# Kernel optimization log

Hardware: AMD Instinct MI355X
Metric: run time of the kernel (lower is better)

The kernel has to match this reference:

```python
import jax, jax.numpy as jnp
import numpy as np

N = 50000      # nodes
E = 400000     # edges (before self loops)
IN = 128       # in_feat
HID = 64       # n_hidden per head
HEADS = [4, 4, 1]
NEG_SLOPE = 0.2  # DGL GATConv default


def gat_layer(h, src, dst, W, al, ar, b, n_nodes):
    # h: [N, Din]; W: [Din, H*F]; al/ar: [H, F]; b: [H*F]
    H, F = al.shape
    feat = (h @ W).reshape(n_nodes, H, F)              # [N,H,F]
    el = jnp.sum(feat * al, axis=-1)                   # [N,H]
    er = jnp.sum(feat * ar, axis=-1)                   # [N,H]
    e = jax.nn.leaky_relu(el[src] + er[dst], NEG_SLOPE)  # [E,H]
    # edge softmax over destination node segments (stable)
    e_max = jax.lax.stop_gradient(jax.ops.segment_max(e, dst, num_segments=n_nodes))
    ex = jnp.exp(e - e_max[dst])                       # [E,H]
    denom = jax.ops.segment_sum(ex, dst, num_segments=n_nodes)  # [N,H]
    alpha = ex / denom[dst]                            # [E,H]
    msg = feat[src] * alpha[:, :, None]                # [E,H,F]
    out = jax.ops.segment_sum(msg, dst, num_segments=n_nodes)   # [N,H,F]
    out = out + b.reshape(1, H, F)
    return out.reshape(n_nodes, H * F)


def setup_inputs() -> dict:
    key = jax.random.key(0)
    ks = jax.random.split(key, 16)
    inp = {
        "node_feat": jax.random.normal(ks[0], (N, IN), jnp.float32),
        "src": jax.random.randint(ks[1], (E,), 0, N),
        "dst": jax.random.randint(ks[2], (E,), 0, N),
    }
    dins = [IN, HID * HEADS[0], HID * HEADS[1]]
    for i, (din, h) in enumerate(zip(dins, HEADS)):
        k = 3 + 3 * i
        inp[f"W{i}"] = jax.random.normal(ks[k], (din, h * HID), jnp.float32) * 0.1
        inp[f"al{i}"] = jax.random.normal(ks[k + 1], (h, HID), jnp.float32) * 0.1
        inp[f"ar{i}"] = jax.random.normal(ks[k + 2], (h, HID), jnp.float32) * 0.1
        inp[f"b{i}"] = jnp.zeros((h * HID,), jnp.float32)
    return inp


def reference(node_feat, src, dst, W0, al0, ar0, b0, W1, al1, ar1, b1, W2, al2, ar2, b2):
    n_nodes = node_feat.shape[0]
    # add_self_loop
    loop = jnp.arange(n_nodes, dtype=src.dtype)
    src_a = jnp.concatenate([src, loop])
    dst_a = jnp.concatenate([dst, loop])
    h = node_feat
    h = gat_layer(h, src_a, dst_a, W0, al0, ar0, b0, n_nodes)  # [N, 4*64]
    h = gat_layer(h, src_a, dst_a, W1, al1, ar1, b1, n_nodes)  # [N, 4*64]
    h = gat_layer(h, src_a, dst_a, W2, al2, ar2, b2, n_nodes)  # [N, 64]
    return h
```

## Files before the change

### kernel.cpp

```cpp
#include <hip/hip_runtime.h>


typedef __attribute__((ext_vector_type(8))) short short8;
typedef __attribute__((ext_vector_type(4))) float f32x4;
typedef __attribute__((ext_vector_type(4))) int int4v;

__device__ __forceinline__ float bf2f(ushort u) {
  union { unsigned int i; float f; } c;
  c.i = ((unsigned int)u) << 16;
  return c.f;
}
__device__ __forceinline__ ushort f2bf(float f) {
  union { float f; unsigned int i; } c;
  c.f = f;
  unsigned int u = c.i;
  u += 0x7FFFu + ((u >> 16) & 1u);
  return (ushort)(u >> 16);
}
__device__ __forceinline__ float lrelu_exp(float x) {
  const float y = fmaxf(x, 0.2f * x);
  return __expf(y);
}
__device__ __forceinline__ void gload_lds16(const ushort* g, void* lds) {
  __builtin_amdgcn_global_load_lds(
      (const __attribute__((address_space(1))) unsigned int*)g,
      (__attribute__((address_space(3))) unsigned int*)lds, 16, 0, 0);
}

__global__ __launch_bounds__(256) void prep_kernel(
    const float* __restrict__ nf, ushort* __restrict__ a0, int n8, int nbA,
    const float* __restrict__ W0, ushort* __restrict__ Wt0,
    const float* __restrict__ W1, ushort* __restrict__ Wt1,
    const float* __restrict__ W2, ushort* __restrict__ Wt2, int nbW,
    int* __restrict__ cnt, int Nn, int nbZ, ushort* __restrict__ feat_sent,
    float* __restrict__ el4, float* __restrict__ el1) {
  const int b = blockIdx.x;
  if (b < nbA) {
    const int i = b * 256 + threadIdx.x;
    if (i >= n8) return;
    const float4 v0 = ((const float4*)nf)[i * 2];
    const float4 v1 = ((const float4*)nf)[i * 2 + 1];
    short8 o;
    o[0] = (short)f2bf(v0.x); o[1] = (short)f2bf(v0.y);
    o[2] = (short)f2bf(v0.z); o[3] = (short)f2bf(v0.w);
    o[4] = (short)f2bf(v1.x); o[5] = (short)f2bf(v1.y);
    o[6] = (short)f2bf(v1.z); o[7] = (short)f2bf(v1.w);
    ((short8*)a0)[i] = o;
  } else if (b < nbA + nbW) {
    const int i = (b - nbA) * 256 + threadIdx.x;
    if (i < 32768) {
      const int k = i >> 8, n = i & 255;
      Wt0[n * 128 + k] = f2bf(W0[i]);
    } else if (i < 32768 + 65536) {
      const int j = i - 32768;
      const int k = j >> 8, n = j & 255;
      Wt1[n * 256 + k] = f2bf(W1[j]);
    } else if (i < 32768 + 65536 + 16384) {
      const int j = i - 32768 - 65536;
      const int k = j >> 6, n = j & 63;
      Wt2[n * 256 + k] = f2bf(W2[j]);
    }
  } else if (b < nbA + nbW + nbZ) {
    const int idx = (b - nbA - nbW) * 256 + threadIdx.x;
    const int base = idx * 4;
    if (base + 4 <= Nn) {
      ((int4v*)cnt)[idx] = (int4v)0;
    } else if (base < Nn) {
      for (int j = base; j < Nn; ++j) cnt[j] = 0;
    }
  } else {
    const int t = threadIdx.x;
    if (t < 128) ((uint*)feat_sent)[t] = 0u;
    if (t >= 128 && t < 132) el4[(size_t)Nn * 4 + (t - 128)] = -1e9f;
    if (t == 132) el1[Nn] = -1e9f;
  }
}

template <int BN, bool FUSE>
__global__ __launch_bounds__(256) void gemm_mfma(
    const ushort* __restrict__ A, const ushort* __restrict__ Wt,
    ushort* __restrict__ C, int M, int K, int Nc,
    const float* __restrict__ al, const float* __restrict__ ar,
    float* __restrict__ el, float* __restrict__ er) {
  constexpr int NF = BN / 32;
  constexpr int NCHB = BN / 8;
  __shared__ ushort As[128][64];
  __shared__ ushort Bs[BN][64];
  const int bm = blockIdx.x * 128;
  const int bn = blockIdx.y * BN;
  const int tid = threadIdx.x;
  const int lane = tid & 63;
  const int wave = tid >> 6;
  const int wm = wave >> 1;
  const int wn = wave & 1;
  const int lrow = lane >> 3;
  const int lslot = lane & 7;

  f32x4 acc[4][NF];
#pragma unroll
  for (int m = 0; m < 4; ++m)
#pragma unroll
    for (int n = 0; n < NF; ++n) acc[m][n] = 0.f;

  for (int k0 = 0; k0 < K; k0 += 64) {
#pragma unroll
    for (int c = wave; c < 16; c += 4) {
      const int row = c * 8 + lrow;
      int rg = bm + row;
      if (rg >= M) rg = M - 1;
      const int kcol = (lslot ^ (row & 7)) * 8;
      gload_lds16(A + (size_t)rg * K + k0 + kcol,
                  (char*)(&As[0][0]) + c * 1024 + lrow * 128 + lslot * 16);
    }
#pragma unroll
    for (int c = wave; c < NCHB; c += 4) {
      const int row = c * 8 + lrow;
      const int kcol = (lslot ^ (row & 7)) * 8;
      gload_lds16(Wt + (size_t)(bn + row) * K + k0 + kcol,
                  (char*)(&Bs[0][0]) + c * 1024 + lrow * 128 + lslot * 16);
    }
    __syncthreads();

#pragma unroll
    for (int kk = 0; kk < 2; ++kk) {
      short8 a[4], b[NF];
#pragma unroll
      for (int m = 0; m < 4; ++m) {
        const int row = wm * 64 + m * 16 + (lane & 15);
        const int slot = (kk * 4 + (lane >> 4)) ^ (row & 7);
        a[m] = *(const short8*)((const char*)&As[0][0] + row * 128 + slot * 16);
      }
#pragma unroll
      for (int n = 0; n < NF; ++n) {
        const int row = wn * (NF * 16) + n * 16 + (lane & 15);
        const int slot = (kk * 4 + (lane >> 4)) ^ (row & 7);
        b[n] = *(const short8*)((const char*)&Bs[0][0] + row * 128 + slot * 16);
      }
#pragma unroll
      for (int m = 0; m < 4; ++m)
#pragma unroll
        for (int n = 0; n < NF; ++n)
          acc[m][n] = __builtin_amdgcn_mfma_f32_16x16x32_bf16(
              a[m], b[n], acc[m][n], 0, 0, 0);
    }
    __syncthreads();
  }

#pragma unroll
  for (int m = 0; m < 4; ++m) {
#pragma unroll
    for (int r = 0; r < 4; ++r) {
      const int row = bm + wm * 64 + m * 16 + (lane >> 4) * 4 + r;
      if (row < M) {
#pragma unroll
        for (int n = 0; n < NF; ++n) {
          const int col = bn + wn * (NF * 16) + n * 16 + (lane & 15);
          C[(size_t)row * Nc + col] = f2bf(acc[m][n][r]);
        }
      }
    }
  }

  if constexpr (FUSE) {
    const int cc = lane & 15;
    const int head = blockIdx.y * 2 + wn;
    float alv[NF], arv[NF];
#pragma unroll
    for (int n = 0; n < NF; ++n) {
      alv[n] = al[head * 64 + n * 16 + cc];
      arv[n] = ar[head * 64 + n * 16 + cc];
    }
#pragma unroll
    for (int m = 0; m < 4; ++m) {
#pragma unroll
      for (int r = 0; r < 4; ++r) {
        float pl = 0.f, pr = 0.f;
#pragma unroll
        for (int n = 0; n < NF; ++n) {
          pl = fmaf(acc[m][n][r], alv[n], pl);
          pr = fmaf(acc[m][n][r], arv[n], pr);
        }
#pragma unroll
        for (int o = 1; o < 16; o <<= 1) {
          pl += __shfl_xor(pl, o);
          pr += __shfl_xor(pr, o);
        }
        if (cc == 0) {
          const int row = bm + wm * 64 + m * 16 + (lane >> 4) * 4 + r;
          if (row < M) {
            el[row * 4 + head] = pl;
            er[row * 4 + head] = pr;
          }
        }
      }
    }
  }
}

__global__ __launch_bounds__(256) void attn_coef_h1(
    const ushort* __restrict__ feat, const float* __restrict__ al,
    const float* __restrict__ ar, float* __restrict__ el,
    float* __restrict__ er, int Nn) {
  const int wid = (blockIdx.x * 256 + threadIdx.x) >> 6;
  const int lane = threadIdx.x & 63;
  const int n = wid * 4 + (lane >> 4);
  const int sub = lane & 15;
  if (n >= Nn) return;
  const short4 v = ((const short4*)(feat + (size_t)n * 64))[sub];
  const float4 a = ((const float4*)al)[sub];
  const float4 r = ((const float4*)ar)[sub];
  const float f0 = bf2f((ushort)v.x), f1 = bf2f((ushort)v.y),
              f2 = bf2f((ushort)v.z), f3 = bf2f((ushort)v.w);
  float pl = f0 * a.x + f1 * a.y + f2 * a.z + f3 * a.w;
  float pr = f0 * r.x + f1 * r.y + f2 * r.z + f3 * r.w;
#pragma unroll
  for (int off = 1; off < 16; off <<= 1) {
    pl += __shfl_xor(pl, off);
    pr += __shfl_xor(pr, off);
  }
  if (sub == 0) {
    el[n] = pl;
    er[n] = pr;
  }
}

__global__ void hist_kernel(const int* __restrict__ dst, int* __restrict__ cnt,
                            int E, int Nn) {
  const int e = blockIdx.x * blockDim.x + threadIdx.x;
  if (e >= E + Nn) return;
  const int d = (e < E) ? dst[e] : (e - E);
  atomicAdd(&cnt[d], 1);
}

__device__ __forceinline__ int block_incl_scan_1024(int x, int* lds16) {
  const int lane = threadIdx.x & 63;
  const int wid = threadIdx.x >> 6;
  int inc = x;
#pragma unroll
  for (int off = 1; off < 64; off <<= 1) {
    const int y = __shfl_up(inc, off);
    if (lane >= off) inc += y;
  }
  if (lane == 63) lds16[wid] = inc;
  __syncthreads();
  if (wid == 0) {
    int t = (lane < 16) ? lds16[lane] : 0;
#pragma unroll
    for (int off = 1; off < 16; off <<= 1) {
      const int y = __shfl_up(t, off);
      if (lane >= off) t += y;
    }
    if (lane < 16) lds16[lane] = t;
  }
  __syncthreads();
  if (wid > 0) inc += lds16[wid - 1];
  return inc;
}

__global__ __launch_bounds__(1024) void scan_blocks_kernel(
    const int* __restrict__ cnt, int* __restrict__ row_ptr,
    int* __restrict__ partials, int n) {
  __shared__ int lds16[16];
  const int i = blockIdx.x * 1024 + threadIdx.x;
  const int x = (i < n) ? ((cnt[i] + 3) & ~3) : 0;
  const int inc = block_incl_scan_1024(x, lds16);
  if (i < n) row_ptr[i] = inc - x;
  if (threadIdx.x == 1023) partials[blockIdx.x] = inc;
}

__global__ __launch_bounds__(1024) void scan_partials_kernel(
    int* __restrict__ partials, int* __restrict__ row_ptr, int nb, int n) {
  __shared__ int lds16[16];
  const int x = (threadIdx.x < nb) ? partials[threadIdx.x] : 0;
  const int inc = block_incl_scan_1024(x, lds16);
  if (threadIdx.x < nb) partials[threadIdx.x] = inc - x;
  if (threadIdx.x == nb - 1) row_ptr[n] = inc;
}

__global__ __launch_bounds__(1024) void add_offsets_kernel(
    int* __restrict__ row_ptr, int* __restrict__ cursor,
    const int* __restrict__ partials, int n) {
  const int i = blockIdx.x * 1024 + threadIdx.x;
  if (i < n) {
    const int v = row_ptr[i] + partials[blockIdx.x];
    row_ptr[i] = v;
    cursor[i] = v;
  }
}

__global__ void scatter_kernel(const int* __restrict__ src,
                               const int* __restrict__ dst,
                               int* __restrict__ cursor, int* __restrict__ esrc,
                               int E, int Nn) {
  const int e = blockIdx.x * blockDim.x + threadIdx.x;
  if (e >= E + Nn) return;
  const int s = (e < E) ? src[e] : (e - E);
  const int d = (e < E) ? dst[e] : (e - E);
  const int pos = atomicAdd(&cursor[d], 1);
  esrc[pos] = s;
}

__global__ void fill_pad_kernel(const int* __restrict__ cursor,
                                const int* __restrict__ row_ptr,
                                int* __restrict__ esrc, int Nn) {
  const int n = blockIdx.x * 256 + threadIdx.x;
  if (n >= Nn) return;
  const int end = row_ptr[n + 1];
  for (int p = cursor[n]; p < end; ++p) esrc[p] = Nn;
}

__global__ __launch_bounds__(256) void agg_fused_h4(
    const int* __restrict__ row_ptr, const int* __restrict__ esrc,
    const float* __restrict__ el, const float* __restrict__ er,
    const ushort* __restrict__ feat, const float* __restrict__ b,
    ushort* __restrict__ out, int Nn) {
  const int n = (blockIdx.x * 256 + threadIdx.x) >> 6;
  const int lane = threadIdx.x & 63;
  if (n >= Nn) return;
  const int h = lane >> 4;
  int i = row_ptr[n];
  const int end = row_ptr[n + 1];
  const float erv = er[n * 4 + h];
  const short4* fb = (const short4*)feat + lane;

  float den = 0.f;
  f32x4 acc = 0.f;
  int s0 = esrc[i], s1 = esrc[i + 1], s2 = esrc[i + 2], s3 = esrc[i + 3];
  float x0 = el[s0 * 4 + h], x1 = el[s1 * 4 + h], x2 = el[s2 * 4 + h],
        x3 = el[s3 * 4 + h];
  short4 f0 = fb[(size_t)s0 * 64], f1 = fb[(size_t)s1 * 64],
         f2 = fb[(size_t)s2 * 64], f3 = fb[(size_t)s3 * 64];
  for (i += 4; i < end; i += 4) {
    const int t0 = esrc[i], t1 = esrc[i + 1], t2 = esrc[i + 2],
              t3 = esrc[i + 3];
    const float y0 = el[t0 * 4 + h], y1 = el[t1 * 4 + h], y2 = el[t2 * 4 + h],
                y3 = el[t3 * 4 + h];
    const short4 g0 = fb[(size_t)t0 * 64], g1 = fb[(size_t)t1 * 64],
                 g2 = fb[(size_t)t2 * 64], g3 = fb[(size_t)t3 * 64];
    const float e0 = lrelu_exp(x0 + erv), e1 = lrelu_exp(x1 + erv),
                e2 = lrelu_exp(x2 + erv), e3 = lrelu_exp(x3 + erv);
    den += (e0 + e1) + (e2 + e3);
    acc[0] += e0 * bf2f((ushort)f0.x) + e1 * bf2f((ushort)f1.x) +
              e2 * bf2f((ushort)f2.x) + e3 * bf2f((ushort)f3.x);
    acc[1] += e0 * bf2f((ushort)f0.y) + e1 * bf2f((ushort)f1.y) +
              e2 * bf2f((ushort)f2.y) + e3 * bf2f((ushort)f3.y);
    acc[2] += e0 * bf2f((ushort)f0.z) + e1 * bf2f((ushort)f1.z) +
              e2 * bf2f((ushort)f2.z) + e3 * bf2f((ushort)f3.z);
    acc[3] += e0 * bf2f((ushort)f0.w) + e1 * bf2f((ushort)f1.w) +
              e2 * bf2f((ushort)f2.w) + e3 * bf2f((ushort)f3.w);
    x0 = y0; x1 = y1; x2 = y2; x3 = y3;
    f0 = g0; f1 = g1; f2 = g2; f3 = g3;
  }
  {
    const float e0 = lrelu_exp(x0 + erv), e1 = lrelu_exp(x1 + erv),
                e2 = lrelu_exp(x2 + erv), e3 = lrelu_exp(x3 + erv);
    den += (e0 + e1) + (e2 + e3);
    acc[0] += e0 * bf2f((ushort)f0.x) + e1 * bf2f((ushort)f1.x) +
              e2 * bf2f((ushort)f2.x) + e3 * bf2f((ushort)f3.x);
    acc[1] += e0 * bf2f((ushort)f0.y) + e1 * bf2f((ushort)f1.y) +
              e2 * bf2f((ushort)f2.y) + e3 * bf2f((ushort)f3.y);
    acc[2] += e0 * bf2f((ushort)f0.z) + e1 * bf2f((ushort)f1.z) +
              e2 * bf2f((ushort)f2.z) + e3 * bf2f((ushort)f3.z);
    acc[3] += e0 * bf2f((ushort)f0.w) + e1 * bf2f((ushort)f1.w) +
              e2 * bf2f((ushort)f2.w) + e3 * bf2f((ushort)f3.w);
  }
  const float rden = 1.f / den;
  const float4 bb = ((const float4*)b)[lane];
  short4 o;
  o.x = (short)f2bf(acc[0] * rden + bb.x);
  o.y = (short)f2bf(acc[1] * rden + bb.y);
  o.z = (short)f2bf(acc[2] * rden + bb.z);
  o.w = (short)f2bf(acc[3] * rden + bb.w);
  ((short4*)out)[(size_t)n * 64 + lane] = o;
}

__global__ __launch_bounds__(256) void agg_fused_h1(
    const int* __restrict__ row_ptr, const int* __restrict__ esrc,
    const float* __restrict__ el, const float* __restrict__ er,
    const ushort* __restrict__ feat, const float* __restrict__ b,
    float* __restrict__ out, int Nn) {
  const int wid = (blockIdx.x * 256 + threadIdx.x) >> 6;
  const int lane = threadIdx.x & 63;
  const int n = wid * 2 + (lane >> 5);
  const int sub = lane & 31;
  if (n >= Nn) return;
  int i = row_ptr[n];
  const int end = row_ptr[n + 1];
  const float erv = er[n];
  const uint* fb = (const uint*)feat + sub;

  float den = 0.f;
  float a0 = 0.f, a1 = 0.f;
  int s0 = esrc[i], s1 = esrc[i + 1], s2 = esrc[i + 2], s3 = esrc[i + 3];
  float x0 = el[s0], x1 = el[s1], x2 = el[s2], x3 = el[s3];
  uint f0 = fb[(size_t)s0 * 32], f1 = fb[(size_t)s1 * 32],
       f2 = fb[(size_t)s2 * 32], f3 = fb[(size_t)s3 * 32];
  for (i += 4; i < end; i += 4) {
    const int t0 = esrc[i], t1 = esrc[i + 1], t2 = esrc[i + 2],
              t3 = esrc[i + 3];
    const float y0 = el[t0], y1 = el[t1], y2 = el[t2], y3 = el[t3];
    const uint g0 = fb[(size_t)t0 * 32], g1 = fb[(size_t)t1 * 32],
               g2 = fb[(size_t)t2 * 32], g3 = fb[(size_t)t3 * 32];
    const float e0 = lrelu_exp(x0 + erv), e1 = lrelu_exp(x1 + erv),
                e2 = lrelu_exp(x2 + erv), e3 = lrelu_exp(x3 + erv);
    den += (e0 + e1) + (e2 + e3);
    a0 += e0 * bf2f((ushort)(f0 & 0xffff)) + e1 * bf2f((ushort)(f1 & 0xffff)) +
          e2 * bf2f((ushort)(f2 & 0xffff)) + e3 * bf2f((ushort)(f3 & 0xffff));
    a1 += e0 * bf2f((ushort)(f0 >> 16)) + e1 * bf2f((ushort)(f1 >> 16)) +
          e2 * bf2f((ushort)(f2 >> 16)) + e3 * bf2f((ushort)(f3 >> 16));
    x0 = y0; x1 = y1; x2 = y2; x3 = y3;
    f0 = g0; f1 = g1; f2 = g2; f3 = g3;
  }
  {
    const float e0 = lrelu_exp(x0 + erv), e1 = lrelu_exp(x1 + erv),
                e2 = lrelu_exp(x2 + erv), e3 = lrelu_exp(x3 + erv);
    den += (e0 + e1) + (e2 + e3);
    a0 += e0 * bf2f((ushort)(f0 & 0xffff)) + e1 * bf2f((ushort)(f1 & 0xffff)) +
          e2 * bf2f((ushort)(f2 & 0xffff)) + e3 * bf2f((ushort)(f3 & 0xffff));
    a1 += e0 * bf2f((ushort)(f0 >> 16)) + e1 * bf2f((ushort)(f1 >> 16)) +
          e2 * bf2f((ushort)(f2 >> 16)) + e3 * bf2f((ushort)(f3 >> 16));
  }
  const float rden = 1.f / den;
  const float2 bb = ((const float2*)b)[sub];
  float2 o;
  o.x = a0 * rden + bb.x;
  o.y = a1 * rden + bb.y;
  ((float2*)out)[(size_t)n * 32 + sub] = o;
}

extern "C" void kernel_launch(void* const* d_in, const int* in_sizes, int n_in,
                              void* d_out, int out_size, void* d_ws,
                              size_t ws_size, hipStream_t stream) {
  const float* nf = (const float*)d_in[0];
  const int* src = (const int*)d_in[1];
  const int* dst = (const int*)d_in[2];
  const float* W0 = (const float*)d_in[3];
  const float* al0 = (const float*)d_in[4];
  const float* ar0 = (const float*)d_in[5];
  const float* b0 = (const float*)d_in[6];
  const float* W1 = (const float*)d_in[7];
  const float* al1 = (const float*)d_in[8];
  const float* ar1 = (const float*)d_in[9];
  const float* b1 = (const float*)d_in[10];
  const float* W2 = (const float*)d_in[11];
  const float* al2 = (const float*)d_in[12];
  const float* ar2 = (const float*)d_in[13];
  const float* b2 = (const float*)d_in[14];

  const int IN = 128;
  const int Nn = in_sizes[0] / IN;
  const int E = in_sizes[1];
  const int ETP = E + 4 * Nn;

  char* ws = (char*)d_ws;
  size_t off = 0;
  auto alloc = [&](size_t bytes) {
    char* p = ws + off;
    off += (bytes + 255) & ~(size_t)255;
    return p;
  };
  ushort* feat = (ushort*)alloc(((size_t)Nn + 1) * 256 * 2);
  ushort* h1 = (ushort*)alloc((size_t)Nn * 256 * 2);
  ushort* h2 = (ushort*)alloc((size_t)Nn * 256 * 2);
  ushort* a0 = (ushort*)alloc((size_t)Nn * 128 * 2);
  ushort* Wt0 = (ushort*)alloc((size_t)256 * 128 * 2);
  ushort* Wt1 = (ushort*)alloc((size_t)256 * 256 * 2);
  ushort* Wt2 = (ushort*)alloc((size_t)64 * 256 * 2);
  float* el4 = (float*)alloc(((size_t)Nn + 1) * 4 * 4);
  float* er4 = (float*)alloc((size_t)Nn * 4 * 4);
  float* el1 = (float*)alloc(((size_t)Nn + 1) * 4);
  float* er1 = (float*)alloc((size_t)Nn * 4);
  int* row_ptr = (int*)alloc(((size_t)Nn + 1) * 4);
  int* cnt = (int*)alloc((size_t)Nn * 4);
  int* cursor = (int*)alloc((size_t)Nn * 4);
  int* esrc = (int*)alloc((size_t)ETP * 4);
  int* partials = (int*)alloc((size_t)1024 * 4);
  (void)ws_size;
  (void)n_in;
  (void)out_size;

  const int n8 = Nn * 16;
  const int nbA = (n8 + 255) / 256;
  const int nbW = (32768 + 65536 + 16384 + 255) / 256;
  const int nbZ = (Nn + 1023) / 1024;
  prep_kernel<<<nbA + nbW + nbZ + 1, 256, 0, stream>>>(
      nf, a0, n8, nbA, W0, Wt0, W1, Wt1, W2, Wt2, nbW, cnt, Nn, nbZ,
      feat + (size_t)Nn * 256, el4, el1);

  const int ET = E + Nn;
  const int nb = (Nn + 1023) / 1024;
  hist_kernel<<<(ET + 255) / 256, 256, 0, stream>>>(dst, cnt, E, Nn);
  scan_blocks_kernel<<<nb, 1024, 0, stream>>>(cnt, row_ptr, partials, Nn);
  scan_partials_kernel<<<1, 1024, 0, stream>>>(partials, row_ptr, nb, Nn);
  add_offsets_kernel<<<nb, 1024, 0, stream>>>(row_ptr, cursor, partials, Nn);
  scatter_kernel<<<(ET + 255) / 256, 256, 0, stream>>>(src, dst, cursor, esrc,
                                                       E, Nn);
  fill_pad_kernel<<<(Nn + 255) / 256, 256, 0, stream>>>(cursor, row_ptr, esrc,
                                                        Nn);

  const int waves_grid = (Nn * 64 + 255) / 256;

  {
    dim3 gg((Nn + 127) / 128, 2);
    gemm_mfma<128, true><<<gg, 256, 0, stream>>>(a0, Wt0, feat, Nn, 128, 256,
                                                 al0, ar0, el4, er4);
    agg_fused_h4<<<waves_grid, 256, 0, stream>>>(row_ptr, esrc, el4, er4, feat,
                                                 b0, h1, Nn);
  }
  {
    dim3 gg((Nn + 127) / 128, 2);
    gemm_mfma<128, true><<<gg, 256, 0, stream>>>(h1, Wt1, feat, Nn, 256, 256,
                                                 al1, ar1, el4, er4);
    agg_fused_h4<<<waves_grid, 256, 0, stream>>>(row_ptr, esrc, el4, er4, feat,
                                                 b1, h2, Nn);
  }
  {
    dim3 gg((Nn + 127) / 128, 1);
    gemm_mfma<64, false><<<gg, 256, 0, stream>>>(h2, Wt2, feat, Nn, 256, 64,
                                                 nullptr, nullptr, nullptr,
                                                 nullptr);
    attn_coef_h1<<<(Nn * 16 + 255) / 256, 256, 0, stream>>>(feat, al2, ar2,
                                                            el1, er1, Nn);
    agg_fused_h1<<<(Nn * 32 + 255) / 256, 256, 0, stream>>>(
        row_ptr, esrc, el1, er1, feat, b2, (float*)d_out, Nn);
  }
}
```

Before: 211.8 us.

## Fuse layer-3 attention coefficients into GEMM, prefill padding, vectorize edge gathers

Three changes. The layer-3 attention coefficients (el/er) are now computed in the GEMM epilogue through an LDS reduction, which removes the attn_coef_h1 kernel. The padding slots in esrc are pre-filled with the sentinel node inside prep_kernel, which removes fill_pad_kernel. The aggregation loops now read edge sources as int4 groups of four and keep two groups in flight to hide more gather latency. Together these save two launches and issue fewer load instructions, at the cost of more registers per thread and an extra LDS sync in the GEMM.

```diff
diff --git a/kernel.cpp b/kernel.cpp
--- a/kernel.cpp
+++ b/kernel.cpp
@@ -32,8 +32,9 @@
     const float* __restrict__ W0, ushort* __restrict__ Wt0,
     const float* __restrict__ W1, ushort* __restrict__ Wt1,
     const float* __restrict__ W2, ushort* __restrict__ Wt2, int nbW,
-    int* __restrict__ cnt, int Nn, int nbZ, ushort* __restrict__ feat_sent,
-    float* __restrict__ el4, float* __restrict__ el1) {
+    int* __restrict__ cnt, int Nn, int nbZ, int* __restrict__ esrc, int ETP,
+    int nbE, ushort* __restrict__ feat_sent, float* __restrict__ el4,
+    float* __restrict__ el1) {
   const int b = blockIdx.x;
   if (b < nbA) {
     const int i = b * 256 + threadIdx.x;
@@ -68,6 +69,14 @@
     } else if (base < Nn) {
       for (int j = base; j < Nn; ++j) cnt[j] = 0;
     }
+  } else if (b < nbA + nbW + nbZ + nbE) {
+    const int idx = (b - nbA - nbW - nbZ) * 256 + threadIdx.x;
+    const int base = idx * 4;
+    if (base + 4 <= ETP) {
+      ((int4*)esrc)[idx] = make_int4(Nn, Nn, Nn, Nn);
+    } else if (base < ETP) {
+      for (int j = base; j < ETP; ++j) esrc[j] = Nn;
+    }
   } else {
     const int t = threadIdx.x;
     if (t < 128) ((uint*)feat_sent)[t] = 0u;
@@ -76,7 +85,7 @@
   }
 }
 
-template <int BN, bool FUSE>
+template <int BN, int FUSE>
 __global__ __launch_bounds__(256) void gemm_mfma(
     const ushort* __restrict__ A, const ushort* __restrict__ Wt,
     ushort* __restrict__ C, int M, int K, int Nc,
@@ -161,7 +170,7 @@
     }
   }
 
-  if constexpr (FUSE) {
+  if constexpr (FUSE == 1) {
     const int cc = lane & 15;
     const int head = blockIdx.y * 2 + wn;
     float alv[NF], arv[NF];
@@ -195,32 +204,47 @@
       }
     }
   }
-}
-
-__global__ __launch_bounds__(256) void attn_coef_h1(
-    const ushort* __restrict__ feat, const float* __restrict__ al,
-    const float* __restrict__ ar, float* __restrict__ el,
-    float* __restrict__ er, int Nn) {
-  const int wid = (blockIdx.x * 256 + threadIdx.x) >> 6;
-  const int lane = threadIdx.x & 63;
-  const int n = wid * 4 + (lane >> 4);
-  const int sub = lane & 15;
-  if (n >= Nn) return;
-  const short4 v = ((const short4*)(feat + (size_t)n * 64))[sub];
-  const float4 a = ((const float4*)al)[sub];
-  const float4 r = ((const float4*)ar)[sub];
-  const float f0 = bf2f((ushort)v.x), f1 = bf2f((ushort)v.y),
-              f2 = bf2f((ushort)v.z), f3 = bf2f((ushort)v.w);
-  float pl = f0 * a.x + f1 * a.y + f2 * a.z + f3 * a.w;
-  float pr = f0 * r.x + f1 * r.y + f2 * r.z + f3 * r.w;
-#pragma unroll
-  for (int off = 1; off < 16; off <<= 1) {
-    pl += __shfl_xor(pl, off);
-    pr += __shfl_xor(pr, off);
-  }
-  if (sub == 0) {
-    el[n] = pl;
-    er[n] = pr;
+
+  if constexpr (FUSE == 2) {
+    float* red = (float*)&As[0][0];
+    const int cc = lane & 15;
+    const int q = lane >> 4;
+    float alv[NF], arv[NF];
+#pragma unroll
+    for (int n = 0; n < NF; ++n) {
+      alv[n] = al[wn * (NF * 16) + n * 16 + cc];
+      arv[n] = ar[wn * (NF * 16) + n * 16 + cc];
+    }
+#pragma unroll
+    for (int m = 0; m < 4; ++m) {
+#pragma unroll
+      for (int r = 0; r < 4; ++r) {
+        float pl = 0.f, pr = 0.f;
+#pragma unroll
+        for (int n = 0; n < NF; ++n) {
+          pl = fmaf(acc[m][n][r], alv[n], pl);
+          pr = fmaf(acc[m][n][r], arv[n], pr);
+        }
+#pragma unroll
+        for (int o = 1; o < 16; o <<= 1) {
+          pl += __shfl_xor(pl, o);
+          pr += __shfl_xor(pr, o);
+        }
+        if (cc == 0) {
+          const int rl = wm * 64 + m * 16 + q * 4 + r;
+          red[rl * 2 + wn] = pl;
+          red[256 + rl * 2 + wn] = pr;
+        }
+      }
+    }
+    __syncthreads();
+    if (tid < 128) {
+      const int row = bm + tid;
+      if (row < M) {
+        el[row] = red[tid * 2] + red[tid * 2 + 1];
+        er[row] = red[256 + tid * 2] + red[256 + tid * 2 + 1];
+      }
+    }
   }
 }
 
@@ -300,13 +324,38 @@
   esrc[pos] = s;
 }
 
-__global__ void fill_pad_kernel(const int* __restrict__ cursor,
-                                const int* __restrict__ row_ptr,
-                                int* __restrict__ esrc, int Nn) {
-  const int n = blockIdx.x * 256 + threadIdx.x;
-  if (n >= Nn) return;
-  const int end = row_ptr[n + 1];
-  for (int p = cursor[n]; p < end; ++p) esrc[p] = Nn;
+struct G4h4 {
+  float x0, x1, x2, x3;
+  short4 f0, f1, f2, f3;
+};
+__device__ __forceinline__ G4h4 ld4_h4(const int* __restrict__ esrc, int p4,
+                                       const float* __restrict__ el, int h,
+                                       const short4* __restrict__ fb) {
+  const int4 s = *(const int4*)(esrc + (p4 << 2));
+  G4h4 g;
+  g.x0 = el[s.x * 4 + h];
+  g.x1 = el[s.y * 4 + h];
+  g.x2 = el[s.z * 4 + h];
+  g.x3 = el[s.w * 4 + h];
+  g.f0 = fb[(size_t)s.x * 64];
+  g.f1 = fb[(size_t)s.y * 64];
+  g.f2 = fb[(size_t)s.z * 64];
+  g.f3 = fb[(size_t)s.w * 64];
+  return g;
+}
+__device__ __forceinline__ void cp4_h4(const G4h4& g, float erv, float& den,
+                                       f32x4& acc) {
+  const float e0 = lrelu_exp(g.x0 + erv), e1 = lrelu_exp(g.x1 + erv),
+              e2 = lrelu_exp(g.x2 + erv), e3 = lrelu_exp(g.x3 + erv);
+  den += (e0 + e1) + (e2 + e3);
+  acc[0] += e0 * bf2f((ushort)g.f0.x) + e1 * bf2f((ushort)g.f1.x) +
+            e2 * bf2f((ushort)g.f2.x) + e3 * bf2f((ushort)g.f3.x);
+  acc[1] += e0 * bf2f((ushort)g.f0.y) + e1 * bf2f((ushort)g.f1.y) +
+            e2 * bf2f((ushort)g.f2.y) + e3 * bf2f((ushort)g.f3.y);
+  acc[2] += e0 * bf2f((ushort)g.f0.z) + e1 * bf2f((ushort)g.f1.z) +
+            e2 * bf2f((ushort)g.f2.z) + e3 * bf2f((ushort)g.f3.z);
+  acc[3] += e0 * bf2f((ushort)g.f0.w) + e1 * bf2f((ushort)g.f1.w) +
+            e2 * bf2f((ushort)g.f2.w) + e3 * bf2f((ushort)g.f3.w);
 }
 
 __global__ __launch_bounds__(256) void agg_fused_h4(
@@ -318,51 +367,35 @@
   const int lane = threadIdx.x & 63;
   if (n >= Nn) return;
   const int h = lane >> 4;
-  int i = row_ptr[n];
-  const int end = row_ptr[n + 1];
+  const int start = row_ptr[n];
+  const int g = (row_ptr[n + 1] - start) >> 2;
+  const int p = start >> 2;
   const float erv = er[n * 4 + h];
   const short4* fb = (const short4*)feat + lane;
 
   float den = 0.f;
   f32x4 acc = 0.f;
-  int s0 = esrc[i], s1 = esrc[i + 1], s2 = esrc[i + 2], s3 = esrc[i + 3];
-  float x0 = el[s0 * 4 + h], x1 = el[s1 * 4 + h], x2 = el[s2 * 4 + h],
-        x3 = el[s3 * 4 + h];
-  short4 f0 = fb[(size_t)s0 * 64], f1 = fb[(size_t)s1 * 64],
-         f2 = fb[(size_t)s2 * 64], f3 = fb[(size_t)s3 * 64];
-  for (i += 4; i < end; i += 4) {
-    const int t0 = esrc[i], t1 = esrc[i + 1], t2 = esrc[i + 2],
-              t3 = esrc[i + 3];
-    const float y0 = el[t0 * 4 + h], y1 = el[t1 * 4 + h], y2 = el[t2 * 4 + h],
-                y3 = el[t3 * 4 + h];
-    const short4 g0 = fb[(size_t)t0 * 64], g1 = fb[(size_t)t1 * 64],
-                 g2 = fb[(size_t)t2 * 64], g3 = fb[(size_t)t3 * 64];
-    const float e0 = lrelu_exp(x0 + erv), e1 = lrelu_exp(x1 + erv),
-                e2 = lrelu_exp(x2 + erv), e3 = lrelu_exp(x3 + erv);
-    den += (e0 + e1) + (e2 + e3);
-    acc[0] += e0 * bf2f((ushort)f0.x) + e1 * bf2f((ushort)f1.x) +
-              e2 * bf2f((ushort)f2.x) + e3 * bf2f((ushort)f3.x);
-    acc[1] += e0 * bf2f((ushort)f0.y) + e1 * bf2f((ushort)f1.y) +
-              e2 * bf2f((ushort)f2.y) + e3 * bf2f((ushort)f3.y);
-    acc[2] += e0 * bf2f((ushort)f0.z) + e1 * bf2f((ushort)f1.z) +
-              e2 * bf2f((ushort)f2.z) + e3 * bf2f((ushort)f3.z);
-    acc[3] += e0 * bf2f((ushort)f0.w) + e1 * bf2f((ushort)f1.w) +
-              e2 * bf2f((ushort)f2.w) + e3 * bf2f((ushort)f3.w);
-    x0 = y0; x1 = y1; x2 = y2; x3 = y3;
-    f0 = g0; f1 = g1; f2 = g2; f3 = g3;
-  }
-  {
-    const float e0 = lrelu_exp(x0 + erv), e1 = lrelu_exp(x1 + erv),
-                e2 = lrelu_exp(x2 + erv), e3 = lrelu_exp(x3 + erv);
-    den += (e0 + e1) + (e2 + e3);
-    acc[0] += e0 * bf2f((ushort)f0.x) + e1 * bf2f((ushort)f1.x) +
-              e2 * bf2f((ushort)f2.x) + e3 * bf2f((ushort)f3.x);
-    acc[1] += e0 * bf2f((ushort)f0.y) + e1 * bf2f((ushort)f1.y) +
-              e2 * bf2f((ushort)f2.y) + e3 * bf2f((ushort)f3.y);
-    acc[2] += e0 * bf2f((ushort)f0.z) + e1 * bf2f((ushort)f1.z) +
-              e2 * bf2f((ushort)f2.z) + e3 * bf2f((ushort)f3.z);
-    acc[3] += e0 * bf2f((ushort)f0.w) + e1 * bf2f((ushort)f1.w) +
-              e2 * bf2f((ushort)f2.w) + e3 * bf2f((ushort)f3.w);
+  G4h4 A = ld4_h4(esrc, p, el, h, fb);
+  if (g == 1) {
+    cp4_h4(A, erv, den, acc);
+  } else {
+    G4h4 B = ld4_h4(esrc, p + 1, el, h, fb);
+    int k = 2;
+    for (; k + 1 < g; k += 2) {
+      cp4_h4(A, erv, den, acc);
+      A = ld4_h4(esrc, p + k, el, h, fb);
+      cp4_h4(B, erv, den, acc);
+      B = ld4_h4(esrc, p + k + 1, el, h, fb);
+    }
+    if (k < g) {
+      cp4_h4(A, erv, den, acc);
+      A = ld4_h4(esrc, p + k, el, h, fb);
+      cp4_h4(B, erv, den, acc);
+      cp4_h4(A, erv, den, acc);
+    } else {
+      cp4_h4(A, erv, den, acc);
+      cp4_h4(B, erv, den, acc);
+    }
   }
   const float rden = 1.f / den;
   const float4 bb = ((const float4*)b)[lane];
@@ -372,6 +405,38 @@
   o.z = (short)f2bf(acc[2] * rden + bb.z);
   o.w = (short)f2bf(acc[3] * rden + bb.w);
   ((short4*)out)[(size_t)n * 64 + lane] = o;
+}
+
+struct G4h1 {
+  float x0, x1, x2, x3;
+  uint f0, f1, f2, f3;
+};
+__device__ __forceinline__ G4h1 ld4_h1(const int* __restrict__ esrc, int p4,
+                                       const float* __restrict__ el,
+                                       const uint* __restrict__ fb) {
+  const int4 s = *(const int4*)(esrc + (p4 << 2));
+  G4h1 g;
+  g.x0 = el[s.x];
+  g.x1 = el[s.y];
+  g.x2 = el[s.z];
+  g.x3 = el[s.w];
+  g.f0 = fb[(size_t)s.x * 32];
+  g.f1 = fb[(size_t)s.y * 32];
+  g.f2 = fb[(size_t)s.z * 32];
+  g.f3 = fb[(size_t)s.w * 32];
+  return g;
+}
+__device__ __forceinline__ void cp4_h1(const G4h1& g, float erv, float& den,
+                                       float& a0, float& a1) {
+  const float e0 = lrelu_exp(g.x0 + erv), e1 = lrelu_exp(g.x1 + erv),
+              e2 = lrelu_exp(g.x2 + erv), e3 = lrelu_exp(g.x3 + erv);
+  den += (e0 + e1) + (e2 + e3);
+  a0 += e0 * bf2f((ushort)(g.f0 & 0xffff)) +
+        e1 * bf2f((ushort)(g.f1 & 0xffff)) +
+        e2 * bf2f((ushort)(g.f2 & 0xffff)) +
+        e3 * bf2f((ushort)(g.f3 & 0xffff));
+  a1 += e0 * bf2f((ushort)(g.f0 >> 16)) + e1 * bf2f((ushort)(g.f1 >> 16)) +
+        e2 * bf2f((ushort)(g.f2 >> 16)) + e3 * bf2f((ushort)(g.f3 >> 16));
 }
 
 __global__ __launch_bounds__(256) void agg_fused_h1(
@@ -384,41 +449,34 @@
   const int n = wid * 2 + (lane >> 5);
   const int sub = lane & 31;
   if (n >= Nn) return;
-  int i = row_ptr[n];
-  const int end = row_ptr[n + 1];
+  const int start = row_ptr[n];
+  const int g = (row_ptr[n + 1] - start) >> 2;
+  const int p = start >> 2;
   const float erv = er[n];
   const uint* fb = (const uint*)feat + sub;
 
-  float den = 0.f;
-  float a0 = 0.f, a1 = 0.f;
-  int s0 = esrc[i], s1 = esrc[i + 1], s2 = esrc[i + 2], s3 = esrc[i + 3];
-  float x0 = el[s0], x1 = el[s1], x2 = el[s2], x3 = el[s3];
-  uint f0 = fb[(size_t)s0 * 32], f1 = fb[(size_t)s1 * 32],
-       f2 = fb[(size_t)s2 * 32], f3 = fb[(size_t)s3 * 32];
-  for (i += 4; i < end; i += 4) {
-    const int t0 = esrc[i], t1 = esrc[i + 1], t2 = esrc[i + 2],
-              t3 = esrc[i + 3];
-    const float y0 = el[t0], y1 = el[t1], y2 = el[t2], y3 = el[t3];
-    const uint g0 = fb[(size_t)t0 * 32], g1 = fb[(size_t)t1 * 32],
-               g2 = fb[(size_t)t2 * 32], g3 = fb[(size_t)t3 * 32];
-    const float e0 = lrelu_exp(x0 + erv), e1 = lrelu_exp(x1 + erv),
-                e2 = lrelu_exp(x2 + erv), e3 = lrelu_exp(x3 + erv);
-    den += (e0 + e1) + (e2 + e3);
-    a0 += e0 * bf2f((ushort)(f0 & 0xffff)) + e1 * bf2f((ushort)(f1 & 0xffff)) +
-          e2 * bf2f((ushort)(f2 & 0xffff)) + e3 * bf2f((ushort)(f3 & 0xffff));
-    a1 += e0 * bf2f((ushort)(f0 >> 16)) + e1 * bf2f((ushort)(f1 >> 16)) +
-          e2 * bf2f((ushort)(f2 >> 16)) + e3 * bf2f((ushort)(f3 >> 16));
-    x0 = y0; x1 = y1; x2 = y2; x3 = y3;
-    f0 = g0; f1 = g1; f2 = g2; f3 = g3;
-  }
-  {
-    const float e0 = lrelu_exp(x0 + erv), e1 = lrelu_exp(x1 + erv),
-                e2 = lrelu_exp(x2 + erv), e3 = lrelu_exp(x3 + erv);
-    den += (e0 + e1) + (e2 + e3);
-    a0 += e0 * bf2f((ushort)(f0 & 0xffff)) + e1 * bf2f((ushort)(f1 & 0xffff)) +
-          e2 * bf2f((ushort)(f2 & 0xffff)) + e3 * bf2f((ushort)(f3 & 0xffff));
-    a1 += e0 * bf2f((ushort)(f0 >> 16)) + e1 * bf2f((ushort)(f1 >> 16)) +
-          e2 * bf2f((ushort)(f2 >> 16)) + e3 * bf2f((ushort)(f3 >> 16));
+  float den = 0.f, a0 = 0.f, a1 = 0.f;
+  G4h1 A = ld4_h1(esrc, p, el, fb);
+  if (g == 1) {
+    cp4_h1(A, erv, den, a0, a1);
+  } else {
+    G4h1 B = ld4_h1(esrc, p + 1, el, fb);
+    int k = 2;
+    for (; k + 1 < g; k += 2) {
+      cp4_h1(A, erv, den, a0, a1);
+      A = ld4_h1(esrc, p + k, el, fb);
+      cp4_h1(B, erv, den, a0, a1);
+      B = ld4_h1(esrc, p + k + 1, el, fb);
+    }
+    if (k < g) {
+      cp4_h1(A, erv, den, a0, a1);
+      A = ld4_h1(esrc, p + k, el, fb);
+      cp4_h1(B, erv, den, a0, a1);
+      cp4_h1(A, erv, den, a0, a1);
+    } else {
+      cp4_h1(A, erv, den, a0, a1);
+      cp4_h1(B, erv, den, a0, a1);
+    }
   }
   const float rden = 1.f / den;
   const float2 bb = ((const float2*)b)[sub];
@@ -483,9 +541,10 @@
   const int nbA = (n8 + 255) / 256;
   const int nbW = (32768 + 65536 + 16384 + 255) / 256;
   const int nbZ = (Nn + 1023) / 1024;
-  prep_kernel<<<nbA + nbW + nbZ + 1, 256, 0, stream>>>(
-      nf, a0, n8, nbA, W0, Wt0, W1, Wt1, W2, Wt2, nbW, cnt, Nn, nbZ,
-      feat + (size_t)Nn * 256, el4, el1);
+  const int nbE = (ETP + 1023) / 1024;
+  prep_kernel<<<nbA + nbW + nbZ + nbE + 1, 256, 0, stream>>>(
+      nf, a0, n8, nbA, W0, Wt0, W1, Wt1, W2, Wt2, nbW, cnt, Nn, nbZ, esrc,
+      ETP, nbE, feat + (size_t)Nn * 256, el4, el1);
 
   const int ET = E + Nn;
   const int nb = (Nn + 1023) / 1024;
@@ -495,32 +554,27 @@
   add_offsets_kernel<<<nb, 1024, 0, stream>>>(row_ptr, cursor, partials, Nn);
   scatter_kernel<<<(ET + 255) / 256, 256, 0, stream>>>(src, dst, cursor, esrc,
                                                        E, Nn);
-  fill_pad_kernel<<<(Nn + 255) / 256, 256, 0, stream>>>(cursor, row_ptr, esrc,
-                                                        Nn);
 
   const int waves_grid = (Nn * 64 + 255) / 256;
 
   {
     dim3 gg((Nn + 127) / 128, 2);
-    gemm_mfma<128, true><<<gg, 256, 0, stream>>>(a0, Wt0, feat, Nn, 128, 256,
-                                                 al0, ar0, el4, er4);
+    gemm_mfma<128, 1><<<gg, 256, 0, stream>>>(a0, Wt0, feat, Nn, 128, 256,
+                                              al0, ar0, el4, er4);
     agg_fused_h4<<<waves_grid, 256, 0, stream>>>(row_ptr, esrc, el4, er4, feat,
                                                  b0, h1, Nn);
   }
   {
     dim3 gg((Nn + 127) / 128, 2);
-    gemm_mfma<128, true><<<gg, 256, 0, stream>>>(h1, Wt1, feat, Nn, 256, 256,
-                                                 al1, ar1, el4, er4);
+    gemm_mfma<128, 1><<<gg, 256, 0, stream>>>(h1, Wt1, feat, Nn, 256, 256,
+                                              al1, ar1, el4, er4);
     agg_fused_h4<<<waves_grid, 256, 0, stream>>>(row_ptr, esrc, el4, er4, feat,
                                                  b1, h2, Nn);
   }
   {
     dim3 gg((Nn + 127) / 128, 1);
-    gemm_mfma<64, false><<<gg, 256, 0, stream>>>(h2, Wt2, feat, Nn, 256, 64,
-                                                 nullptr, nullptr, nullptr,
-                                                 nullptr);
-    attn_coef_h1<<<(Nn * 16 + 255) / 256, 256, 0, stream>>>(feat, al2, ar2,
-                                                            el1, er1, Nn);
+    gemm_mfma<64, 2><<<gg, 256, 0, stream>>>(h2, Wt2, feat, Nn, 256, 64, al2,
+                                             ar2, el1, er1);
     agg_fused_h1<<<(Nn * 32 + 255) / 256, 256, 0, stream>>>(
         row_ptr, esrc, el1, er1, feat, b2, (float*)d_out, Nn);
   }
```

New measurement: 223.1 us. +5.3%, slower.
